# Kernel optimization log

Hardware: AMD Instinct MI355X
Metric: run time of the kernel (lower is better)

## Reference

```python
import jax, jax.numpy as jnp
import numpy as np
import math
from jax import lax

B, L, D, P, V, K = 4, 2048, 512, 128, 8, 4


def _lin(x, w, b):
    # torch Linear: y = x @ W^T + b, W shape (out, in)
    return jnp.einsum('...i,oi->...o', x, w) + b


def _gelu(v):
    return jax.nn.gelu(v, approximate=False)


def _dwconv_causal(x_ncl, w, b):
    # depthwise causal conv: torch Conv1d(groups=D, padding=K-1) then [:, :, :L]
    y = lax.conv_general_dilated(x_ncl, w, (1,), [(K - 1, 0)],
                                 dimension_numbers=('NCH', 'OIH', 'NCH'),
                                 feature_group_count=D)
    return y + b[None, :, None]


def _ln(v, g, b):
    m = v.mean(-1, keepdims=True)
    var = v.var(-1, keepdims=True)
    return (v - m) / jnp.sqrt(var + 1e-5) * g + b


def setup_inputs() -> dict:
    key = jax.random.key(0)
    it = iter(jax.random.split(key, 64))
    def nrm(shape, s=0.02):
        return jax.random.normal(next(it), shape, dtype=jnp.float32) * s
    z = lambda *s: jnp.zeros(s, jnp.float32)
    return dict(
        x=nrm((B, L, D), 1.0),
        lc_w=nrm((D, 1, K)), lc_b=z(D),
        cg_w=nrm((D, 1, K)), cg_b=z(D),
        cp_w=nrm((D, D)), cp_b=z(D),
        tw_w=nrm((D, D)), tw_b=z(D),
        omega_scale=jnp.full((D,), 0.01, jnp.float32),
        pi0_w=nrm((D, D)), pi0_b=z(D),
        pi2_w=nrm((D, D)), pi2_b=z(D),
        m1v_w=nrm((D, D)), m1v_b=z(D),
        m1o_w=nrm((D, D)), m1o_b=z(D),
        mag_w=nrm((D, D)), mag_b=z(D),
        mag_scale=jnp.asarray(5.0, jnp.float32),
        qo_w=nrm((D, D)), qo_b=z(D),
        ke_w=nrm((P, D)), ke_b=z(P),
        ve_w=nrm((V, D)), ve_b=z(V),
        sk0_w=nrm((D, 2 * D)), sk0_b=z(D),
        sk2_w=nrm((P, D)), sk2_b=z(P),
        sg_w=nrm((1, D)), sg_b=z(1),
        kvo_w=nrm((D, V)), kvo_b=z(D),
        ln_g=jnp.ones(5 * D, jnp.float32), ln_b=z(5 * D),
        o1_w=nrm((2 * D, 5 * D)), o1_b=z(2 * D),
        o2_w=nrm((D, 2 * D)), o2_b=z(D),
    )


def reference(x, lc_w, lc_b, cg_w, cg_b, cp_w, cp_b, tw_w, tw_b, omega_scale,
              pi0_w, pi0_b, pi2_w, pi2_b, m1v_w, m1v_b, m1o_w, m1o_b,
              mag_w, mag_b, mag_scale, qo_w, qo_b, ke_w, ke_b, ve_w, ve_b,
              sk0_w, sk0_b, sk2_w, sk2_b, sg_w, sg_b, kvo_w, kvo_b,
              ln_g, ln_b, o1_w, o1_b, o2_w, o2_b):
    Bs, Ls, Ds = x.shape
    # local gated causal depthwise conv branch
    xc = jnp.transpose(x, (0, 2, 1))                          # (B, D, L)
    co = _dwconv_causal(xc, lc_w, lc_b)
    cg = jax.nn.sigmoid(_dwconv_causal(xc, cg_w, cg_b))
    conv_out = _lin(jnp.transpose(co * cg, (0, 2, 1)), cp_w, cp_b)
    # evolving phases
    omega_scaled = _lin(x, tw_w, tw_b) * jnp.abs(omega_scale)
    phi = _lin(_gelu(_lin(x, pi0_w, pi0_b)), pi2_w, pi2_b) + jnp.cumsum(omega_scaled, axis=1)
    cos_phi = jnp.cos(phi)
    sin_phi = jnp.sin(phi)
    # magnitude-weighted phase memory
    v1 = _lin(x, m1v_w, m1v_b)
    magnitude = jax.nn.sigmoid(_lin(x, mag_w, mag_b)) * jnp.abs(mag_scale)
    wv1 = magnitude * v1
    sqrt_mag = jnp.sqrt(jnp.cumsum(magnitude, axis=1) + 1e-8)
    mem1_cos = jnp.cumsum(wv1 * cos_phi, axis=1) / sqrt_mag
    mem1_sin = jnp.cumsum(wv1 * sin_phi, axis=1) / sqrt_mag
    phi_q = phi + _lin(x, qo_w, qo_b)
    pos_ret = (mem1_cos * jnp.cos(phi_q) + mem1_sin * jnp.sin(phi_q)) / math.sqrt(Ds)
    pos_out = _lin(pos_ret, m1o_w, m1o_b)
    # phase-keyed associative KV memory
    query_phase = jnp.tanh(_lin(x, ke_w, ke_b)) * math.pi    # (B, L, P)
    values = _lin(x, ve_w, ve_b)                              # (B, L, V)
    store_gate = jax.nn.sigmoid(_lin(x, sg_w, sg_b))          # (B, L, 1)
    positions = jnp.arange(1, Ls + 1, dtype=x.dtype).reshape(1, -1, 1)
    context_avg = jnp.cumsum(x, axis=1) / positions
    storage_phase = jnp.tanh(_lin(_gelu(_lin(jnp.concatenate([x, context_avg], -1), sk0_w, sk0_b)), sk2_w, sk2_b)) * math.pi
    gated_vals = values * store_gate                          # (B, L, V)
    kv_mem_cos = jnp.cumsum(jnp.cos(storage_phase)[..., None] * gated_vals[:, :, None, :], axis=1)
    kv_mem_sin = jnp.cumsum(jnp.sin(storage_phase)[..., None] * gated_vals[:, :, None, :], axis=1)
    gate_norm = jnp.sqrt(jnp.maximum(jnp.cumsum(store_gate, axis=1), 1.0))[..., None]  # (B, L, 1, 1)
    kv_mem_cos = kv_mem_cos / gate_norm
    kv_mem_sin = kv_mem_sin / gate_norm
    kv_retrieved = (jnp.cos(query_phase)[..., None] * kv_mem_cos +
                    jnp.sin(query_phase)[..., None] * kv_mem_sin).sum(axis=2) / math.sqrt(P)
    kv_out = _lin(kv_retrieved, kvo_w, kvo_b)
    # combine (dropout is identity in eval)
    combined = jnp.concatenate([conv_out, pos_out, kv_out, x * cos_phi, x * sin_phi], axis=-1)
    h = _ln(combined, ln_g, ln_b)
    h = _lin(_gelu(_lin(h, o1_w, o1_b)), o2_w, o2_b)
    return x + h
```

## Files before the change

### kernel.cpp

```cpp
#include <hip/hip_runtime.h>
#include <cstdint>

typedef unsigned short u16;
typedef short short8 __attribute__((ext_vector_type(8)));
typedef float floatx4 __attribute__((ext_vector_type(4)));

#define B_ 4
#define L_ 2048
#define D_ 512
#define P_ 128
#define V_ 8
#define BL (B_ * L_)
#define NC_ 256
#define CH_ 8
#define PI_F 3.14159265358979323846f

__device__ inline u16 f2b(float f) {
    unsigned u = __float_as_uint(f);
    unsigned r = u + 0x7FFFu + ((u >> 16) & 1u);
    return (u16)(r >> 16);
}
__device__ inline float b2f(u16 h) {
    return __uint_as_float(((unsigned)h) << 16);
}
__device__ inline float gelu_f(float v) {
    return 0.5f * v * (1.0f + erff(v * 0.70710678118654752f));
}
__device__ inline float sigm(float v) {
    return 1.0f / (1.0f + __expf(-v));
}
__device__ inline float tanh_fast(float v) {
    return 1.0f - 2.0f / (1.0f + __expf(2.0f * v));
}

__device__ inline void async16(const u16* g, u16* l) {
    __builtin_amdgcn_global_load_lds(
        (const __attribute__((address_space(1))) unsigned int*)g,
        (__attribute__((address_space(3))) unsigned int*)l, 16, 0, 0);
}

extern __shared__ u16 smem_dyn[];

enum { EPI_F32 = 0, EPI_BF16 = 1, EPI_GELU_BF16 = 2, EPI_RESID_F32 = 3,
       EPI_PASS1 = 4, EPI_ATOMIC = 5 };

template <int EPI>
__device__ __forceinline__ void gemm_body(
    const u16* __restrict__ A, int lda,
    const u16* __restrict__ W, int ldw,
    const float* __restrict__ bias,
    void* __restrict__ Cout, int ldc, int N, int K,
    const float* __restrict__ resid, int mt, int nt)
{
    const int tid  = threadIdx.x;
    const int lane = tid & 63;
    const int wid  = tid >> 6;
    const int wm   = wid & 1, wn = wid >> 1;
    const int l16  = lane & 15, quad = lane >> 4;
    const int rswz = (l16 >> 1) & 3;

    floatx4 acc[4][2] = {};

    const u16* Ab = A + (size_t)(mt * 128) * lda;
    const u16* Wb = W + (size_t)(nt * 128) * ldw;

    const int srow = lane >> 2;
    const int scol = ((lane & 3) ^ ((srow >> 1) & 3)) * 8;
    const u16* ga0 = Ab + (size_t)(wid * 16 + srow) * lda + scol;
    const u16* gb0 = Wb + (size_t)(wid * 16 + srow) * ldw + scol;
    const int lW = wid * 512;

    const int nsteps = K >> 5;

    auto stage = [&](int t, int s) {
        u16* base = smem_dyn + s * 8192;
        const int ko = t * 32;
        async16(ga0 + ko, base + lW);
        async16(gb0 + ko, base + 4096 + lW);
    };

    auto readfrag = [&](int slot, short8 (&a)[4], short8 (&b)[2]) {
        const u16* As = smem_dyn + slot * 8192;
        const u16* Bs = As + 4096;
#pragma unroll
        for (int i = 0; i < 4; i++)
            a[i] = *(const short8*)(&As[(wm * 64 + i * 16 + l16) * 32 + (quad ^ rswz) * 8]);
#pragma unroll
        for (int j = 0; j < 2; j++)
            b[j] = *(const short8*)(&Bs[(wn * 32 + j * 16 + l16) * 32 + (quad ^ rswz) * 8]);
    };

    auto mfma8 = [&](short8 (&a)[4], short8 (&b)[2]) {
        __builtin_amdgcn_s_setprio(1);
#pragma unroll
        for (int i = 0; i < 4; i++)
#pragma unroll
            for (int j = 0; j < 2; j++)
                acc[i][j] = __builtin_amdgcn_mfma_f32_16x16x32_bf16(a[i], b[j], acc[i][j], 0, 0, 0);
        __builtin_amdgcn_s_setprio(0);
    };

    stage(0, 0);
    if (nsteps > 1) stage(1, 1);
    if (nsteps > 2) stage(2, 2);
    if (nsteps > 2)      asm volatile("s_waitcnt vmcnt(4)" ::: "memory");
    else if (nsteps > 1) asm volatile("s_waitcnt vmcnt(2)" ::: "memory");
    else                 asm volatile("s_waitcnt vmcnt(0)" ::: "memory");
    __builtin_amdgcn_s_barrier();
    asm volatile("" ::: "memory");

    short8 aE[4], bE[2], aO[4], bO[2];
    readfrag(0, aE, bE);

    for (int t = 0; t < nsteps; t += 2) {
        asm volatile("s_waitcnt lgkmcnt(0)" ::: "memory");
        if (t + 2 < nsteps)      asm volatile("s_waitcnt vmcnt(2)" ::: "memory");
        else if (t + 1 < nsteps) asm volatile("s_waitcnt vmcnt(0)" ::: "memory");
        __builtin_amdgcn_s_barrier();
        asm volatile("" ::: "memory");
        if (t + 3 < nsteps) stage(t + 3, t % 3);
        if (t + 1 < nsteps) readfrag((t + 1) % 3, aO, bO);
        mfma8(aE, bE);
        const int t1 = t + 1;
        asm volatile("s_waitcnt lgkmcnt(0)" ::: "memory");
        if (t1 + 2 < nsteps)      asm volatile("s_waitcnt vmcnt(2)" ::: "memory");
        else if (t1 + 1 < nsteps) asm volatile("s_waitcnt vmcnt(0)" ::: "memory");
        __builtin_amdgcn_s_barrier();
        asm volatile("" ::: "memory");
        if (t1 + 3 < nsteps) stage(t1 + 3, t1 % 3);
        if (t1 + 1 < nsteps) readfrag((t1 + 1) % 3, aE, bE);
        mfma8(aO, bO);
    }

#pragma unroll
    for (int i = 0; i < 4; i++) {
#pragma unroll
        for (int j = 0; j < 2; j++) {
#pragma unroll
            for (int r = 0; r < 4; r++) {
                int grow = mt * 128 + wm * 64 + i * 16 + quad * 4 + r;
                int gcol = nt * 128 + wn * 32 + j * 16 + l16;
                if (gcol < N) {
                    float v = acc[i][j][r] + (bias ? bias[gcol] : 0.0f);
                    size_t off = (size_t)grow * ldc + gcol;
                    if (EPI == EPI_F32)            ((float*)Cout)[off] = v;
                    else if (EPI == EPI_BF16)      ((u16*)Cout)[off] = f2b(v);
                    else if (EPI == EPI_GELU_BF16) ((u16*)Cout)[off] = f2b(gelu_f(v));
                    else if (EPI == EPI_PASS1) {
                        float vv = (gcol >= 512 && gcol < 1024) ? gelu_f(v) : v;
                        ((u16*)Cout)[off] = f2b(vv);
                    }
                    else if (EPI == EPI_RESID_F32) ((float*)Cout)[off] = v + resid[off];
                    else                           atomicAdd(&((float*)Cout)[off], v);
                }
            }
        }
    }
}

template <int EPI>
__global__ __launch_bounds__(512)
void gemm256(const u16* __restrict__ A, int lda,
             const u16* __restrict__ W, int ldw,
             const float* __restrict__ bias,
             void* __restrict__ C, int ldc, int N, int K,
             const float* __restrict__ resid)
{
    int kz = blockIdx.z;
    gemm_body<EPI>(A + (size_t)kz * K, lda, W + (size_t)kz * K, ldw,
                   kz == 0 ? bias : nullptr, C, ldc, N, K, resid,
                   blockIdx.x, blockIdx.y);
}

__global__ __launch_bounds__(512)
void mega1(const u16* __restrict__ xcat, const u16* __restrict__ convg,
           const u16* __restrict__ wcat1, const float* __restrict__ bcat1,
           const u16* __restrict__ kesgw, const float* __restrict__ kesgb,
           const u16* __restrict__ cpw, const float* __restrict__ cp_b,
           u16* __restrict__ out1, float* __restrict__ kesgo, u16* __restrict__ combined)
{
    int y = blockIdx.y, mt = blockIdx.x;
    if (y < 20)
        gemm_body<EPI_PASS1>(xcat, 1024, wcat1, 512, bcat1, out1, 2560, 2560, 512, nullptr, mt, y);
    else if (y < 22)
        gemm_body<EPI_F32>(xcat, 1024, kesgw, 512, kesgb, kesgo, 144, 144, 512, nullptr, mt, y - 20);
    else
        gemm_body<EPI_BF16>(convg, 512, cpw, 512, cp_b, combined, 2560, 512, 512, nullptr, mt, y - 22);
}

__global__ __launch_bounds__(512)
void mega2(const u16* __restrict__ posret, const u16* __restrict__ xcat,
           const u16* __restrict__ m1ow, const float* __restrict__ m1o_b,
           const u16* __restrict__ sk0w, const float* __restrict__ sk0_b,
           u16* __restrict__ combined, u16* __restrict__ sk0g)
{
    int y = blockIdx.y, mt = blockIdx.x;
    if (y < 4)
        gemm_body<EPI_BF16>(posret, 512, m1ow, 512, m1o_b, combined + 512, 2560, 512, 512, nullptr, mt, y);
    else
        gemm_body<EPI_GELU_BF16>(xcat, 1024, sk0w, 1024, sk0_b, sk0g, 512, 512, 1024, nullptr, mt, y - 4);
}

__global__ __launch_bounds__(256)
void prep_weights(const float* tw, const float* pi0, const float* m1v, const float* mag, const float* qo,
                  const float* ke, const float* ve, const float* sg,
                  const float* pi2, const float* cp, const float* sk0, const float* sk2,
                  const float* m1o, const float* o1, const float* o2,
                  const float* tw_b, const float* pi0_b, const float* m1v_b, const float* mag_b, const float* qo_b,
                  const float* ke_b, const float* ve_b, const float* sg_b,
                  u16* wcat1, float* bcat1, u16* kesgw, float* kesgb,
                  u16* pi2w, u16* cpw, u16* sk0w, u16* sk2w, u16* m1ow, u16* o1w, u16* o2w)
{
    int idx = blockIdx.x * 256 + threadIdx.x;
    const int n0 = 2560 * 512;
    const int n1 = n0 + 256 * 512;
    const int n2 = n1 + 512 * 512;
    const int n3 = n2 + 512 * 512;
    const int n4 = n3 + 512 * 1024;
    const int n5 = n4 + 128 * 512;
    const int n6 = n5 + 512 * 512;
    const int n7 = n6 + 1024 * 2560;
    const int n8 = n7 + 512 * 1024;
    const int n9 = n8 + 2560;
    const int n10 = n9 + 256;
    if (idx < n0) {
        int r = idx >> 9, k = idx & 511;
        const float* s = (r < 512) ? tw : (r < 1024) ? pi0 : (r < 1536) ? m1v : (r < 2048) ? mag : qo;
        wcat1[idx] = f2b(s[(r & 511) * 512 + k]);
    } else if (idx < n1) {
        int i = idx - n0; int r = i >> 9, k = i & 511;
        float v;
        if (r < 128)      v = ke[r * 512 + k];
        else if (r < 136) v = ve[(r - 128) * 512 + k];
        else if (r == 136) v = sg[k];
        else               v = 0.0f;
        kesgw[i] = f2b(v);
    }
    else if (idx < n2) { int i = idx - n1; pi2w[i] = f2b(pi2[i]); }
    else if (idx < n3) { int i = idx - n2; cpw[i]  = f2b(cp[i]); }
    else if (idx < n4) { int i = idx - n3; sk0w[i] = f2b(sk0[i]); }
    else if (idx < n5) { int i = idx - n4; sk2w[i] = f2b(sk2[i]); }
    else if (idx < n6) { int i = idx - n5; m1ow[i] = f2b(m1o[i]); }
    else if (idx < n7) { int i = idx - n6; o1w[i]  = f2b(o1[i]); }
    else if (idx < n8) { int i = idx - n7; o2w[i]  = f2b(o2[i]); }
    else if (idx < n9) {
        int i = idx - n8;
        const float* s = (i < 512) ? tw_b : (i < 1024) ? pi0_b : (i < 1536) ? m1v_b : (i < 2048) ? mag_b : qo_b;
        bcat1[i] = s[i & 511];
    } else if (idx < n10) {
        int i = idx - n9;
        kesgb[i] = (i < 128) ? ke_b[i] : (i < 136) ? ve_b[i - 128] : (i == 136) ? sg_b[0] : 0.0f;
    }
}

__global__ __launch_bounds__(256)
void conv_gate(const float* __restrict__ x,
               const float* __restrict__ lcw, const float* __restrict__ lcb,
               const float* __restrict__ cgw, const float* __restrict__ cgb,
               u16* __restrict__ out, u16* __restrict__ xcat)
{
    int idx = blockIdx.x * 256 + threadIdx.x;
    int d = idx & 511; int bl = idx >> 9;
    int l = bl & (L_ - 1); int b = bl >> 11;
    float a0 = 0.f, a1 = 0.f, xv3 = 0.f;
#pragma unroll
    for (int k = 0; k < 4; k++) {
        int ls = l - 3 + k;
        if (ls >= 0) {
            float xv = x[((size_t)(b * L_ + ls)) * 512 + d];
            if (k == 3) xv3 = xv;
            a0 += xv * lcw[d * 4 + k];
            a1 += xv * cgw[d * 4 + k];
        }
    }
    a0 += lcb[d];
    a1 = sigm(a1 + cgb[d]);
    out[idx] = f2b(a0 * a1);
    xcat[(size_t)bl * 1024 + d] = f2b(xv3);
}

__device__ __forceinline__ void scan_a_body(
    int blk, const u16* __restrict__ out1, const float* __restrict__ x,
    const float* __restrict__ oscale, const float* __restrict__ msc,
    float* __restrict__ cs_o, float* __restrict__ cs_x, float* __restrict__ cs_m)
{
    int nc = blk & 15, dt = (blk >> 4) & 7, b = blk >> 7;
    int t = threadIdx.x; int dl = t & 63, lg = t >> 6;
    int d = dt * 64 + dl;
    float os = fabsf(oscale[d]);
    float ms = fabsf(msc[0]);
    float so = 0.f, sx = 0.f, sm = 0.f;
    int l0 = nc * 128 + lg * 16;
    for (int i = 0; i < 16; i++) {
        size_t r = (size_t)(b * L_ + l0 + i);
        so += b2f(out1[r * 2560 + d]) * os;
        sm += sigm(b2f(out1[r * 2560 + 1536 + d])) * ms;
        sx += x[r * 512 + d];
    }
    __shared__ float sh[3][8][64];
    sh[0][lg][dl] = so; sh[1][lg][dl] = sx; sh[2][lg][dl] = sm;
    __syncthreads();
    if (t < 64) {
        float a = 0.f, xx = 0.f, m = 0.f;
        for (int g = 0; g < 8; g++) { a += sh[0][g][t]; xx += sh[1][g][t]; m += sh[2][g][t]; }
        size_t o = ((size_t)(b * 16 + nc)) * 512 + dt * 64 + t;
        cs_o[o] = a; cs_x[o] = xx; cs_m[o] = m;
    }
}

__device__ __forceinline__ void gate_body(const float* __restrict__ kesgo,
                                          float* __restrict__ gni)
{
    if (threadIdx.x >= 256) return;
    int b = threadIdx.x >> 6; int lane = threadIdx.x & 63;
    float v[32]; float s = 0.f;
#pragma unroll
    for (int i = 0; i < 32; i++) {
        int l = lane * 32 + i;
        v[i] = sigm(kesgo[((size_t)(b * L_ + l)) * 144 + 136]);
        s += v[i];
    }
    float sc = s;
#pragma unroll
    for (int ofs = 1; ofs < 64; ofs <<= 1) {
        float t = __shfl_up(sc, ofs, 64);
        if (lane >= ofs) sc += t;
    }
    float run = sc - s;
#pragma unroll
    for (int i = 0; i < 32; i++) {
        run += v[i];
        gni[b * L_ + lane * 32 + i] = rsqrtf(fmaxf(run, 1.0f));
    }
}

__global__ __launch_bounds__(512)
void stage2(const u16* __restrict__ out1, const u16* __restrict__ pi2w,
            const float* __restrict__ pi2_b, u16* __restrict__ phib,
            const float* __restrict__ x, const float* __restrict__ oscale,
            const float* __restrict__ msc,
            float* __restrict__ cs_o, float* __restrict__ cs_x, float* __restrict__ cs_m,
            const float* __restrict__ kesgo, float* __restrict__ gni)
{
    int blk = blockIdx.x;
    if (blk < 256)
        gemm_body<EPI_BF16>(out1 + 512, 2560, pi2w, 512, pi2_b, phib, 512, 512, 512,
                            nullptr, blk & 63, blk >> 6);
    else if (blk < 768)
        scan_a_body(blk - 256, out1, x, oscale, msc, cs_o, cs_x, cs_m);
    else
        gate_body(kesgo, gni);
}

__global__ __launch_bounds__(512)
void scan_c(const u16* __restrict__ out1, const u16* __restrict__ phib,
            const float* __restrict__ oscale, const float* __restrict__ msc,
            const float* __restrict__ cs_o,
            float* __restrict__ phi, float* __restrict__ cs_wc, float* __restrict__ cs_ws)
{
    int blk = blockIdx.x;
    int nc = blk & 15, dt = (blk >> 4) & 7, b = blk >> 7;
    int t = threadIdx.x; int dl = t & 63, lg = t >> 6;
    int d = dt * 64 + dl;
    float os = fabsf(oscale[d]);
    float ms = fabsf(msc[0]);
    int l0 = nc * 128 + lg * 16;
    float so = 0.f;
    for (int i = 0; i < 16; i++) {
        size_t r = (size_t)(b * L_ + l0 + i);
        so += b2f(out1[r * 2560 + d]) * os;
    }
    __shared__ float sh[8][64];
    __shared__ float shw[2][8][64];
    sh[lg][dl] = so;
    __syncthreads();
    float pre = 0.f;
    for (int p = 0; p < nc; p++) pre += cs_o[((size_t)(b * 16 + p)) * 512 + d];
    for (int g = 0; g < lg; g++) pre += sh[g][dl];
    float cum = pre, swc = 0.f, sws = 0.f;
    for (int i = 0; i < 16; i++) {
        size_t r = (size_t)(b * L_ + l0 + i);
        cum += b2f(out1[r * 2560 + d]) * os;
        float ph = b2f(phib[r * 512 + d]) + cum;
        phi[r * 512 + d] = ph;
        float mg = sigm(b2f(out1[r * 2560 + 1536 + d])) * ms;
        float wv = mg * b2f(out1[r * 2560 + 1024 + d]);
        float s = __sinf(ph), c = __cosf(ph);
        swc += wv * c; sws += wv * s;
    }
    shw[0][lg][dl] = swc; shw[1][lg][dl] = sws;
    __syncthreads();
    if (t < 64) {
        float a = 0.f, bb = 0.f;
        for (int g = 0; g < 8; g++) { a += shw[0][g][t]; bb += shw[1][g][t]; }
        size_t o = ((size_t)(b * 16 + nc)) * 512 + dt * 64 + t;
        cs_wc[o] = a; cs_ws[o] = bb;
    }
}

__global__ __launch_bounds__(512)
void scan_e(const u16* __restrict__ out1, const float* __restrict__ phi,
            const float* __restrict__ x, const float* __restrict__ msc,
            const float* __restrict__ cs_m, const float* __restrict__ cs_x,
            const float* __restrict__ cs_wc, const float* __restrict__ cs_ws,
            u16* __restrict__ posret, u16* __restrict__ xcat, u16* __restrict__ combined)
{
    int blk = blockIdx.x;
    int nc = blk & 15, dt = (blk >> 4) & 7, b = blk >> 7;
    int t = threadIdx.x; int dl = t & 63, lg = t >> 6;
    int d = dt * 64 + dl;
    float ms = fabsf(msc[0]);
    int l0 = nc * 128 + lg * 16;
    float sm = 0.f, swc = 0.f, sws = 0.f, sx = 0.f;
    for (int i = 0; i < 16; i++) {
        size_t r = (size_t)(b * L_ + l0 + i);
        float ph = phi[r * 512 + d];
        float mg = sigm(b2f(out1[r * 2560 + 1536 + d])) * ms;
        float wv = mg * b2f(out1[r * 2560 + 1024 + d]);
        float s = __sinf(ph), c = __cosf(ph);
        sm += mg; swc += wv * c; sws += wv * s; sx += x[r * 512 + d];
    }
    __shared__ float sh[4][8][64];
    sh[0][lg][dl] = sm; sh[1][lg][dl] = swc; sh[2][lg][dl] = sws; sh[3][lg][dl] = sx;
    __syncthreads();
    float cm = 0.f, cwc = 0.f, cws = 0.f, cx = 0.f;
    for (int p = 0; p < nc; p++) {
        size_t o = ((size_t)(b * 16 + p)) * 512 + d;
        cm += cs_m[o]; cwc += cs_wc[o]; cws += cs_ws[o]; cx += cs_x[o];
    }
    for (int g = 0; g < lg; g++) {
        cm += sh[0][g][dl]; cwc += sh[1][g][dl]; cws += sh[2][g][dl]; cx += sh[3][g][dl];
    }
    const float invsqD = 0.044194173824159216f;
    for (int i = 0; i < 16; i++) {
        int l = l0 + i;
        size_t r = (size_t)(b * L_ + l);
        float ph = phi[r * 512 + d];
        float mg = sigm(b2f(out1[r * 2560 + 1536 + d])) * ms;
        float wv = mg * b2f(out1[r * 2560 + 1024 + d]);
        float xv = x[r * 512 + d];
        float s = __sinf(ph), c = __cosf(ph);
        cm += mg; cwc += wv * c; cws += wv * s; cx += xv;
        float smag = sqrtf(cm + 1e-8f);
        float m1c = cwc / smag, m1s = cws / smag;
        float phq = ph + b2f(out1[r * 2560 + 2048 + d]);
        float sq = __sinf(phq), cq = __cosf(phq);
        float pr = (m1c * cq + m1s * sq) * invsqD;
        posret[r * 512 + d] = f2b(pr);
        xcat[r * 1024 + 512 + d] = f2b(cx / (float)(l + 1));
        combined[r * 2560 + 1536 + d] = f2b(xv * c);
        combined[r * 2560 + 2048 + d] = f2b(xv * s);
    }
}

__global__ __launch_bounds__(64)
void kv_chunk(const float* __restrict__ sppre, const float* __restrict__ kesgo,
              float* __restrict__ spc, float* __restrict__ sps,
              float* __restrict__ csum)
{
    int blk = blockIdx.x; int nc = blk & (NC_ - 1), b = blk >> 8;
    int t = threadIdx.x;
    float Sc[2][8] = {}, Ss[2][8] = {};
    for (int i = 0; i < CH_; i++) {
        size_t r = (size_t)(b * L_ + nc * CH_ + i);
        float sgate = sigm(kesgo[r * 144 + 136]);
        float g[8];
#pragma unroll
        for (int v = 0; v < 8; v++) g[v] = kesgo[r * 144 + 128 + v] * sgate;
#pragma unroll
        for (int j = 0; j < 2; j++) {
            int p = t + j * 64;
            float sp = tanh_fast(sppre[r * 128 + p]) * PI_F;
            float s = __sinf(sp), c = __cosf(sp);
            spc[r * 128 + p] = c; sps[r * 128 + p] = s;
#pragma unroll
            for (int v = 0; v < 8; v++) { Sc[j][v] += c * g[v]; Ss[j][v] += s * g[v]; }
        }
    }
    size_t base = (size_t)blk * 2048;
#pragma unroll
    for (int j = 0; j < 2; j++)
#pragma unroll
        for (int v = 0; v < 8; v++) {
            csum[base + (t + j * 64) * 8 + v]        = Sc[j][v];
            csum[base + 1024 + (t + j * 64) * 8 + v] = Ss[j][v];
        }
}

__global__ __launch_bounds__(256)
void kv_scan(const float* __restrict__ cin, float* __restrict__ cex)
{
    int t = blockIdx.x * 256 + threadIdx.x;
    int pv = t & 1023; int cs = (t >> 10) & 1; int b = t >> 11;
    float run = 0.f;
    for (int nc = 0; nc < NC_; nc++) {
        size_t o = ((size_t)(b * NC_ + nc)) * 2048 + cs * 1024 + pv;
        cex[o] = run; run += cin[o];
    }
}

__global__ __launch_bounds__(64)
void kv_retrieve(const float* __restrict__ spc, const float* __restrict__ sps,
                 const float* __restrict__ kesgo,
                 const float* __restrict__ gni, const float* __restrict__ cex,
                 const float* __restrict__ kvo_w, const float* __restrict__ kvo_b,
                 u16* __restrict__ combined)
{
    int blk = blockIdx.x; int nc = blk & (NC_ - 1), b = blk >> 8;
    int t = threadIdx.x;
    const int nb = t * 8;
    float wr[8][8], br[8];
#pragma unroll
    for (int n = 0; n < 8; n++) {
        *(float4*)&wr[n][0] = *(const float4*)&kvo_w[(nb + n) * 8];
        *(float4*)&wr[n][4] = *(const float4*)&kvo_w[(nb + n) * 8 + 4];
        br[n] = kvo_b[nb + n];
    }
    float Sc[2][8], Ss[2][8];
    size_t base = (size_t)blk * 2048;
#pragma unroll
    for (int j = 0; j < 2; j++)
#pragma unroll
        for (int v = 0; v < 8; v++) {
            Sc[j][v] = cex[base + (t + j * 64) * 8 + v];
            Ss[j][v] = cex[base + 1024 + (t + j * 64) * 8 + v];
        }
    for (int i = 0; i < CH_; i++) {
        size_t r = (size_t)(b * L_ + nc * CH_ + i);
        float sgate = sigm(kesgo[r * 144 + 136]);
        float g[8];
#pragma unroll
        for (int v = 0; v < 8; v++) g[v] = kesgo[r * 144 + 128 + v] * sgate;
        float part[8];
#pragma unroll
        for (int v = 0; v < 8; v++) part[v] = 0.f;
#pragma unroll
        for (int j = 0; j < 2; j++) {
            int p = t + j * 64;
            float c = spc[r * 128 + p], s = sps[r * 128 + p];
#pragma unroll
            for (int v = 0; v < 8; v++) { Sc[j][v] += c * g[v]; Ss[j][v] += s * g[v]; }
            float qp = tanh_fast(kesgo[r * 144 + p]) * PI_F;
            float sq = __sinf(qp), cq = __cosf(qp);
#pragma unroll
            for (int v = 0; v < 8; v++) part[v] += cq * Sc[j][v] + sq * Ss[j][v];
        }
#pragma unroll
        for (int ofs = 1; ofs < 64; ofs <<= 1)
#pragma unroll
            for (int v = 0; v < 8; v++) part[v] += __shfl_xor(part[v], ofs, 64);
        float scale = gni[r] * 0.08838834764831845f;
        float pv[8];
#pragma unroll
        for (int v = 0; v < 8; v++) pv[v] = part[v] * scale;
        u16 outv[8];
#pragma unroll
        for (int n = 0; n < 8; n++) {
            float a = br[n];
#pragma unroll
            for (int v = 0; v < 8; v++) a += pv[v] * wr[n][v];
            outv[n] = f2b(a);
        }
        *(uint4*)&combined[r * 2560 + 1024 + nb] = *(const uint4*)outv;
    }
}

__global__ __launch_bounds__(320)
void ln_rows(u16* __restrict__ combined, const float* __restrict__ g, const float* __restrict__ bb)
{
    size_t m = blockIdx.x; int t = threadIdx.x;
    u16 vv[8];
    *(uint4*)vv = *(const uint4*)&combined[m * 2560 + t * 8];
    float f[8]; float s = 0.f, s2 = 0.f;
#pragma unroll
    for (int k = 0; k < 8; k++) { f[k] = b2f(vv[k]); s += f[k]; s2 += f[k] * f[k]; }
#pragma unroll
    for (int ofs = 1; ofs < 64; ofs <<= 1) {
        s  += __shfl_xor(s, ofs, 64);
        s2 += __shfl_xor(s2, ofs, 64);
    }
    __shared__ float shs[5], shs2[5];
    int wv = t >> 6;
    if ((t & 63) == 0) { shs[wv] = s; shs2[wv] = s2; }
    __syncthreads();
    float S = 0.f, S2 = 0.f;
#pragma unroll
    for (int i = 0; i < 5; i++) { S += shs[i]; S2 += shs2[i]; }
    float mean = S * (1.0f / 2560.0f);
    float var  = S2 * (1.0f / 2560.0f) - mean * mean;
    float rstd = rsqrtf(var + 1e-5f);
#pragma unroll
    for (int k = 0; k < 8; k++) {
        int c = t * 8 + k;
        vv[k] = f2b((f[k] - mean) * rstd * g[c] + bb[c]);
    }
    *(uint4*)&combined[m * 2560 + t * 8] = *(const uint4*)vv;
}

extern "C" void kernel_launch(void* const* d_in, const int* in_sizes, int n_in,
                              void* d_out, int out_size, void* d_ws, size_t ws_size,
                              hipStream_t stream)
{
    const float* x     = (const float*)d_in[0];
    const float* lc_w  = (const float*)d_in[1];
    const float* lc_b  = (const float*)d_in[2];
    const float* cg_w  = (const float*)d_in[3];
    const float* cg_b  = (const float*)d_in[4];
    const float* cp_w  = (const float*)d_in[5];
    const float* cp_b  = (const float*)d_in[6];
    const float* tw_w  = (const float*)d_in[7];
    const float* tw_b  = (const float*)d_in[8];
    const float* omega_scale = (const float*)d_in[9];
    const float* pi0_w = (const float*)d_in[10];
    const float* pi0_b = (const float*)d_in[11];
    const float* pi2_w = (const float*)d_in[12];
    const float* pi2_b = (const float*)d_in[13];
    const float* m1v_w = (const float*)d_in[14];
    const float* m1v_b = (const float*)d_in[15];
    const float* m1o_w = (const float*)d_in[16];
    const float* m1o_b = (const float*)d_in[17];
    const float* mag_w = (const float*)d_in[18];
    const float* mag_b = (const float*)d_in[19];
    const float* mag_scale = (const float*)d_in[20];
    const float* qo_w  = (const float*)d_in[21];
    const float* qo_b  = (const float*)d_in[22];
    const float* ke_w  = (const float*)d_in[23];
    const float* ke_b  = (const float*)d_in[24];
    const float* ve_w  = (const float*)d_in[25];
    const float* ve_b  = (const float*)d_in[26];
    const float* sk0_w = (const float*)d_in[27];
    const float* sk0_b = (const float*)d_in[28];
    const float* sk2_w = (const float*)d_in[29];
    const float* sk2_b = (const float*)d_in[30];
    const float* sg_w  = (const float*)d_in[31];
    const float* sg_b  = (const float*)d_in[32];
    const float* kvo_w = (const float*)d_in[33];
    const float* kvo_b = (const float*)d_in[34];
    const float* ln_g  = (const float*)d_in[35];
    const float* ln_b  = (const float*)d_in[36];
    const float* o1_w  = (const float*)d_in[37];
    const float* o1_b  = (const float*)d_in[38];
    const float* o2_w  = (const float*)d_in[39];
    const float* o2_b  = (const float*)d_in[40];
    float* out = (float*)d_out;

    char* base = (char*)d_ws;
    size_t off = 0;
    auto alloc = [&](size_t bytes) -> void* {
        void* p = base + off;
        off += (bytes + 255) & ~(size_t)255;
        return p;
    };

    u16*   wcat1  = (u16*)  alloc((size_t)2560 * 512 * 2);
    float* bcat1  = (float*)alloc(2560 * 4);
    u16*   kesgw  = (u16*)  alloc((size_t)256 * 512 * 2);
    float* kesgb  = (float*)alloc(256 * 4);
    u16*   pi2w   = (u16*)  alloc((size_t)512 * 512 * 2);
    u16*   cpw    = (u16*)  alloc((size_t)512 * 512 * 2);
    u16*   sk0w   = (u16*)  alloc((size_t)512 * 1024 * 2);
    u16*   sk2w   = (u16*)  alloc((size_t)128 * 512 * 2);
    u16*   m1ow   = (u16*)  alloc((size_t)512 * 512 * 2);
    u16*   o1w    = (u16*)  alloc((size_t)1024 * 2560 * 2);
    u16*   o2w    = (u16*)  alloc((size_t)512 * 1024 * 2);
    u16*   xcat   = (u16*)  alloc((size_t)BL * 1024 * 2);
    u16*   out1   = (u16*)  alloc((size_t)BL * 2560 * 2);
    u16*   phib   = (u16*)  alloc((size_t)BL * 512 * 2);
    float* phi    = (float*)alloc((size_t)BL * 512 * 4);
    float* kesgo  = (float*)alloc((size_t)BL * 144 * 4);
    u16*   convg  = (u16*)  alloc((size_t)BL * 512 * 2);
    float* sppre  = (float*)alloc((size_t)BL * 128 * 4);
    u16*   combined = (u16*)alloc((size_t)BL * 2560 * 2);
    float* cs_o   = (float*)alloc((size_t)4 * 16 * 512 * 4);
    float* cs_x   = (float*)alloc((size_t)4 * 16 * 512 * 4);
    float* cs_m   = (float*)alloc((size_t)4 * 16 * 512 * 4);
    float* cs_wc  = (float*)alloc((size_t)4 * 16 * 512 * 4);
    float* cs_ws  = (float*)alloc((size_t)4 * 16 * 512 * 4);
    float* gni    = (float*)alloc((size_t)BL * 4);
    u16*   posret = convg;
    u16*   sk0g   = out1;
    float* spc    = phi;
    float* sps    = phi + (size_t)BL * 128;
    float* kvcs   = (float*)phib;
    float* kvex   = phi + (size_t)BL * 256;
    u16*   o1g    = xcat;
    (void)ws_size; (void)in_sizes; (void)n_in; (void)out_size;

    const size_t SMEM = 49152;

    prep_weights<<<23307, 256, 0, stream>>>(
        tw_w, pi0_w, m1v_w, mag_w, qo_w, ke_w, ve_w, sg_w,
        pi2_w, cp_w, sk0_w, sk2_w, m1o_w, o1_w, o2_w,
        tw_b, pi0_b, m1v_b, mag_b, qo_b, ke_b, ve_b, sg_b,
        wcat1, bcat1, kesgw, kesgb, pi2w, cpw, sk0w, sk2w, m1ow, o1w, o2w);
    conv_gate<<<16384, 256, 0, stream>>>(x, lc_w, lc_b, cg_w, cg_b, convg, xcat);
    mega1<<<dim3(64, 26), 512, SMEM, stream>>>(xcat, convg, wcat1, bcat1,
                                               kesgw, kesgb, cpw, cp_b,
                                               out1, kesgo, combined);
    stage2<<<769, 512, SMEM, stream>>>(out1, pi2w, pi2_b, phib,
                                       x, omega_scale, mag_scale,
                                       cs_o, cs_x, cs_m, kesgo, gni);
    scan_c<<<512, 512, 0, stream>>>(out1, phib, omega_scale, mag_scale, cs_o,
                                    phi, cs_wc, cs_ws);
    scan_e<<<512, 512, 0, stream>>>(out1, phi, x, mag_scale, cs_m, cs_x, cs_wc, cs_ws,
                                    posret, xcat, combined);
    mega2<<<dim3(64, 8), 512, SMEM, stream>>>(posret, xcat, m1ow, m1o_b,
                                              sk0w, sk0_b, combined, sk0g);
    hipMemsetAsync(sppre, 0, (size_t)BL * 128 * 4, stream);
    gemm256<EPI_ATOMIC><<<dim3(64, 1, 4), 512, SMEM, stream>>>(sk0g, 512, sk2w, 512, sk2_b,
                                                               sppre, 128, 128, 128, nullptr);
    kv_chunk<<<4 * NC_, 64, 0, stream>>>(sppre, kesgo, spc, sps, kvcs);
    kv_scan<<<32, 256, 0, stream>>>(kvcs, kvex);
    kv_retrieve<<<4 * NC_, 64, 0, stream>>>(spc, sps, kesgo, gni, kvex, kvo_w, kvo_b, combined);
    ln_rows<<<8192, 320, 0, stream>>>(combined, ln_g, ln_b);
    gemm256<EPI_GELU_BF16><<<dim3(64, 8), 512, SMEM, stream>>>(combined, 2560, o1w, 2560, o1_b,
                                                               o1g, 1024, 1024, 2560, nullptr);
    gemm256<EPI_RESID_F32><<<dim3(64, 4), 512, SMEM, stream>>>(o1g, 1024, o2w, 1024, o2_b,
                                                               out, 512, 512, 1024, x);
}
```

Measured before the change: 505.5 us.

## Parallelize KV chunk scan across groups and vectorize causal conv gate

The serial kv_scan, which ran 8192 threads each walking 256 chunks, is split into two kernels. The first computes per-group partial sums over 8 groups. The second adds the earlier groups' partials and scans within its group, giving 8x more threads and shorter serial chains at the cost of an extra launch and re-reading the chunk sums. Separately, conv_gate now handles 4 channels per thread with float4 loads and 64-bit bf16 stores, cutting the thread count and memory transactions.

```diff
diff --git a/kernel.cpp b/kernel.cpp
--- a/kernel.cpp
+++ b/kernel.cpp
@@ -13,6 +13,7 @@
 #define BL (B_ * L_)
 #define NC_ 256
 #define CH_ 8
+#define NG_ 8
 #define PI_F 3.14159265358979323846f
 
 __device__ inline u16 f2b(float f) {
@@ -260,23 +261,39 @@
                u16* __restrict__ out, u16* __restrict__ xcat)
 {
     int idx = blockIdx.x * 256 + threadIdx.x;
-    int d = idx & 511; int bl = idx >> 9;
+    int d4 = (idx & 127) * 4; int bl = idx >> 7;
     int l = bl & (L_ - 1); int b = bl >> 11;
-    float a0 = 0.f, a1 = 0.f, xv3 = 0.f;
+    float4 xr[4];
+#pragma unroll
+    for (int k = 0; k < 4; k++) xr[k] = make_float4(0.f, 0.f, 0.f, 0.f);
 #pragma unroll
     for (int k = 0; k < 4; k++) {
         int ls = l - 3 + k;
-        if (ls >= 0) {
-            float xv = x[((size_t)(b * L_ + ls)) * 512 + d];
-            if (k == 3) xv3 = xv;
-            a0 += xv * lcw[d * 4 + k];
-            a1 += xv * cgw[d * 4 + k];
-        }
-    }
-    a0 += lcb[d];
-    a1 = sigm(a1 + cgb[d]);
-    out[idx] = f2b(a0 * a1);
-    xcat[(size_t)bl * 1024 + d] = f2b(xv3);
+        if (ls >= 0)
+            xr[k] = *(const float4*)&x[((size_t)(b * L_ + ls)) * 512 + d4];
+    }
+    float4 lw[4], cw[4];
+#pragma unroll
+    for (int j = 0; j < 4; j++) {
+        lw[j] = *(const float4*)&lcw[(d4 + j) * 4];
+        cw[j] = *(const float4*)&cgw[(d4 + j) * 4];
+    }
+    float4 lb = *(const float4*)&lcb[d4];
+    float4 cb = *(const float4*)&cgb[d4];
+    u16 outv[4], xcv[4];
+#pragma unroll
+    for (int j = 0; j < 4; j++) {
+        float xk0 = (&xr[0].x)[j], xk1 = (&xr[1].x)[j],
+              xk2 = (&xr[2].x)[j], xk3 = (&xr[3].x)[j];
+        float a0 = (&lb.x)[j] + xk0 * (&lw[j].x)[0] + xk1 * (&lw[j].x)[1]
+                              + xk2 * (&lw[j].x)[2] + xk3 * (&lw[j].x)[3];
+        float a1 = sigm((&cb.x)[j] + xk0 * (&cw[j].x)[0] + xk1 * (&cw[j].x)[1]
+                                   + xk2 * (&cw[j].x)[2] + xk3 * (&cw[j].x)[3]);
+        outv[j] = f2b(a0 * a1);
+        xcv[j]  = f2b(xk3);
+    }
+    *(uint2*)&out[(size_t)bl * 512 + d4]         = *(const uint2*)outv;
+    *(uint2*)&xcat[(size_t)bl * 1024 + d4]       = *(const uint2*)xcv;
 }
 
 __device__ __forceinline__ void scan_a_body(
@@ -488,12 +505,31 @@
 }
 
 __global__ __launch_bounds__(256)
-void kv_scan(const float* __restrict__ cin, float* __restrict__ cex)
+void kv_scan_p(const float* __restrict__ cin, float* __restrict__ part)
 {
     int t = blockIdx.x * 256 + threadIdx.x;
-    int pv = t & 1023; int cs = (t >> 10) & 1; int b = t >> 11;
+    int pv = t & 1023; int cs = (t >> 10) & 1; int g = (t >> 11) & (NG_ - 1);
+    int b = t >> 14;
+    float s = 0.f;
+    for (int i = 0; i < NC_ / NG_; i++) {
+        int nc = g * (NC_ / NG_) + i;
+        s += cin[((size_t)(b * NC_ + nc)) * 2048 + cs * 1024 + pv];
+    }
+    part[((size_t)((b * 2 + cs) * NG_ + g)) * 1024 + pv] = s;
+}
+
+__global__ __launch_bounds__(256)
+void kv_scan_f(const float* __restrict__ cin, const float* __restrict__ part,
+               float* __restrict__ cex)
+{
+    int t = blockIdx.x * 256 + threadIdx.x;
+    int pv = t & 1023; int cs = (t >> 10) & 1; int g = (t >> 11) & (NG_ - 1);
+    int b = t >> 14;
     float run = 0.f;
-    for (int nc = 0; nc < NC_; nc++) {
+    for (int gp = 0; gp < g; gp++)
+        run += part[((size_t)((b * 2 + cs) * NG_ + gp)) * 1024 + pv];
+    for (int i = 0; i < NC_ / NG_; i++) {
+        int nc = g * (NC_ / NG_) + i;
         size_t o = ((size_t)(b * NC_ + nc)) * 2048 + cs * 1024 + pv;
         cex[o] = run; run += cin[o];
     }
@@ -677,6 +713,7 @@
     float* cs_wc  = (float*)alloc((size_t)4 * 16 * 512 * 4);
     float* cs_ws  = (float*)alloc((size_t)4 * 16 * 512 * 4);
     float* gni    = (float*)alloc((size_t)BL * 4);
+    float* kvpart = (float*)alloc((size_t)B_ * 2 * NG_ * 1024 * 4);
     u16*   posret = convg;
     u16*   sk0g   = out1;
     float* spc    = phi;
@@ -693,7 +730,7 @@
         pi2_w, cp_w, sk0_w, sk2_w, m1o_w, o1_w, o2_w,
         tw_b, pi0_b, m1v_b, mag_b, qo_b, ke_b, ve_b, sg_b,
         wcat1, bcat1, kesgw, kesgb, pi2w, cpw, sk0w, sk2w, m1ow, o1w, o2w);
-    conv_gate<<<16384, 256, 0, stream>>>(x, lc_w, lc_b, cg_w, cg_b, convg, xcat);
+    conv_gate<<<4096, 256, 0, stream>>>(x, lc_w, lc_b, cg_w, cg_b, convg, xcat);
     mega1<<<dim3(64, 26), 512, SMEM, stream>>>(xcat, convg, wcat1, bcat1,
                                                kesgw, kesgb, cpw, cp_b,
                                                out1, kesgo, combined);
@@ -710,7 +747,8 @@
     gemm256<EPI_ATOMIC><<<dim3(64, 1, 4), 512, SMEM, stream>>>(sk0g, 512, sk2w, 512, sk2_b,
                                                                sppre, 128, 128, 128, nullptr);
     kv_chunk<<<4 * NC_, 64, 0, stream>>>(sppre, kesgo, spc, sps, kvcs);
-    kv_scan<<<32, 256, 0, stream>>>(kvcs, kvex);
+    kv_scan_p<<<256, 256, 0, stream>>>(kvcs, kvpart);
+    kv_scan_f<<<256, 256, 0, stream>>>(kvcs, kvpart, kvex);
     kv_retrieve<<<4 * NC_, 64, 0, stream>>>(spc, sps, kesgo, gni, kvex, kvo_w, kvo_b, combined);
     ln_rows<<<8192, 320, 0, stream>>>(combined, ln_g, ln_b);
     gemm256<EPI_GELU_BF16><<<dim3(64, 8), 512, SMEM, stream>>>(combined, 2560, o1w, 2560, o1_b,
```

Result: faster. 485.0 us (-4.0%).
